# Optimization experiments

Measured on AMD Instinct MI355X. Metric: run time of the kernel, lower is better.

The kernel has to match this reference:

```python
import jax, jax.numpy as jnp
import numpy as np
from jax import lax

N_STEPS = 8          # fixed-step discretization of t in [0, 1]
GN_GROUPS = 32       # group_norm(width) -> GroupNorm(min(32, width), width)
GN_EPS = 1e-5

# Tsit5 Butcher tableau (c nodes, a stage coeffs, b solution weights; b7 = 0)
_C = (0.161, 0.327, 0.9, 0.9800255409045097, 1.0)
_A = (
    (0.161,),
    (-0.008480655492356989, 0.335480655492357),
    (2.8971530571054935, -6.359448489975075, 4.3622954328695815),
    (5.325864828439257, -11.748883564062828, 7.4955393428898365, -0.09249506636175525),
    (5.86145544294642, -12.92096931784711, 8.159367898576159, -0.071584973281401, -0.028269050394068383),
)
_B = (0.09646076681806523, 0.01, 0.4798896504144996, 1.379008574103742, -3.290069515436081, 2.324710524099774)


def _conv3x3(x, w, b):
    # x: [B, Cin, H, W], w: [Cout, Cin, 3, 3], padding=1, stride=1
    y = lax.conv_general_dilated(x, w, (1, 1), ((1, 1), (1, 1)),
                                 dimension_numbers=("NCHW", "OIHW", "NCHW"))
    return y + b[None, :, None, None]


def _group_norm(x, scale, bias):
    B, C, H, W = x.shape
    xr = x.reshape(B, GN_GROUPS, C // GN_GROUPS, H, W)
    mu = xr.mean(axis=(2, 3, 4), keepdims=True)
    var = xr.var(axis=(2, 3, 4), keepdims=True)
    xn = ((xr - mu) * lax.rsqrt(var + GN_EPS)).reshape(B, C, H, W)
    return xn * scale[None, :, None, None] + bias[None, :, None, None]


def _ode_func(t, x, p):
    # ConcatConv2D: prepend a channel filled with scalar t
    B, _, H, W = x.shape
    tt = jnp.full((B, 1, H, W), t, dtype=x.dtype)
    h = _conv3x3(jnp.concatenate([tt, x], axis=1), p["conv1_w"], p["conv1_b"])
    h = jax.nn.relu(_group_norm(h, p["gn1_scale"], p["gn1_bias"]))
    tt2 = jnp.full((B, 1, H, W), t, dtype=x.dtype)
    h = _conv3x3(jnp.concatenate([tt2, h], axis=1), p["conv2_w"], p["conv2_b"])
    return _group_norm(h, p["gn2_scale"], p["gn2_bias"])


def _tsit5_solve(x, p):
    dt = jnp.float32(1.0 / N_STEPS)

    def step(carry, _):
        y, t = carry
        k1 = _ode_func(t, y, p)
        k2 = _ode_func(t + _C[0] * dt, y + dt * (_A[0][0] * k1), p)
        k3 = _ode_func(t + _C[1] * dt, y + dt * (_A[1][0] * k1 + _A[1][1] * k2), p)
        k4 = _ode_func(t + _C[2] * dt,
                       y + dt * (_A[2][0] * k1 + _A[2][1] * k2 + _A[2][2] * k3), p)
        k5 = _ode_func(t + _C[3] * dt,
                       y + dt * (_A[3][0] * k1 + _A[3][1] * k2 + _A[3][2] * k3 + _A[3][3] * k4), p)
        k6 = _ode_func(t + _C[4] * dt,
                       y + dt * (_A[4][0] * k1 + _A[4][1] * k2 + _A[4][2] * k3
                                 + _A[4][3] * k4 + _A[4][4] * k5), p)
        y_next = y + dt * (_B[0] * k1 + _B[1] * k2 + _B[2] * k3
                           + _B[3] * k4 + _B[4] * k5 + _B[5] * k6)
        return (y_next, t + dt), None

    (yT, _), _ = lax.scan(step, (x, jnp.float32(0.0)), None, length=N_STEPS)
    return yT


def setup_inputs() -> dict:
    key = jax.random.key(0)
    ks = jax.random.split(key, 5)
    B, C, H, W = 64, 64, 32, 32
    cin = C + 1  # concat t channel
    fan_in = cin * 9
    lim = 1.0 / np.sqrt(fan_in)
    x = jax.random.normal(ks[0], (B, C, H, W), dtype=jnp.float32)
    conv1_w = jax.random.uniform(ks[1], (C, cin, 3, 3), jnp.float32, -lim, lim)
    conv1_b = jax.random.uniform(ks[2], (C,), jnp.float32, -lim, lim)
    conv2_w = jax.random.uniform(ks[3], (C, cin, 3, 3), jnp.float32, -lim, lim)
    conv2_b = jax.random.uniform(ks[4], (C,), jnp.float32, -lim, lim)
    return {
        "x": x,
        "conv1_w": conv1_w, "conv1_b": conv1_b,
        "gn1_scale": jnp.ones((C,), jnp.float32), "gn1_bias": jnp.zeros((C,), jnp.float32),
        "conv2_w": conv2_w, "conv2_b": conv2_b,
        "gn2_scale": jnp.ones((C,), jnp.float32), "gn2_bias": jnp.zeros((C,), jnp.float32),
    }


def reference(x, conv1_w, conv1_b, gn1_scale, gn1_bias, conv2_w, conv2_b, gn2_scale, gn2_bias):
    p = {"conv1_w": conv1_w, "conv1_b": conv1_b, "gn1_scale": gn1_scale, "gn1_bias": gn1_bias,
         "conv2_w": conv2_w, "conv2_b": conv2_b, "gn2_scale": gn2_scale, "gn2_bias": gn2_bias}
    return _tsit5_solve(x, p)
```

## Files before the change

### kernel.cpp

```cpp
#include <hip/hip_runtime.h>

typedef __attribute__((ext_vector_type(8))) _Float16 f16x8;
typedef __attribute__((ext_vector_type(4))) float f32x4;
typedef unsigned short u16;

#define BB 64
#define NPIX 1024
#define NELEM (BB*64*NPIX)
#define NRT 8

#define PLANE (6*34*64)

__device__ __forceinline__ int swz8(int c8, int p) {
    return (c8 + ((p + (p >> 2)) & 7)) & 7;
}

__device__ __forceinline__ u16 f2h(float x) {
    _Float16 h = (_Float16)x;
    return __builtin_bit_cast(u16, h);
}
__device__ __forceinline__ float h2f(u16 u) {
    return (float)__builtin_bit_cast(_Float16, u);
}

__global__ __launch_bounds__(256) void prep_w_k(
    const float* __restrict__ w, u16* __restrict__ wt)
{
    int t = blockIdx.x*256 + threadIdx.x;
    if (t >= 4608) return;
    int lane = t & 63;
    int f = t >> 6;
    int g = f & 7;
    int tap = f >> 3;
    int coutblk = g & 3;
    int kc = g >> 2;
    int cout = coutblk*16 + (lane & 15);
    int quad = lane >> 4;
    u16 v[8];
#pragma unroll
    for (int j = 0; j < 8; ++j) {
        int cin = kc*32 + quad*8 + j;
        v[j] = f2h(w[((size_t)cout*65 + (cin+1))*9 + tap]);
    }
    u16* dst = wt + ((size_t)tap*4096 + (g*64 + lane)*8);
    *(ushort4*)(dst)     = make_ushort4(v[0], v[1], v[2], v[3]);
    *(ushort4*)(dst + 4) = make_ushort4(v[4], v[5], v[6], v[7]);
}

__global__ __launch_bounds__(256) void smap_k(
    const float* __restrict__ w, float* __restrict__ smap)
{
    int t = blockIdx.x*256 + threadIdx.x;
    int cout = t >> 10;
    int pix = t & 1023;
    int y = pix >> 5, x = pix & 31;
    float s = 0.f;
#pragma unroll
    for (int dy = 0; dy < 3; ++dy)
#pragma unroll
        for (int dx = 0; dx < 3; ++dx) {
            int yy = y + dy - 1, xx = x + dx - 1;
            if ((unsigned)yy < 32u && (unsigned)xx < 32u)
                s += w[(size_t)cout*65*9 + dy*3 + dx];
        }
    smap[t] = s;
}

template<int MODE, int NK, bool WRITEY>
__global__ __launch_bounds__(512, 4) void conv_mfma_k(
    const float* __restrict__ src0, const u16* __restrict__ srcb,
    const u16* __restrict__ kp0, const u16* __restrict__ kp1,
    const u16* __restrict__ kp2, const u16* __restrict__ kp3,
    const u16* __restrict__ kp4, const u16* __restrict__ kp5,
    float* __restrict__ yout,
    float* __restrict__ part,
    const float* __restrict__ gns, const float* __restrict__ gnb,
    const float* __restrict__ gks, const float* __restrict__ gkb,
    const u16* __restrict__ wt, const float* __restrict__ smap,
    const float* __restrict__ bias, u16* __restrict__ out, float tval,
    int slot_in, int slot_out,
    float a1, float a2, float a3, float a4, float a5, float a6)
{
    __shared__ u16 lds_in[PLANE];
    __shared__ float kaf[6][64];
    __shared__ float kbf[64];
    __shared__ float ps[256], pss[256];
    __shared__ float rg[64], rgq[64];

    const int rt  = blockIdx.x;
    const int b   = blockIdx.y;
    const int tid = threadIdx.x;
    const int wv   = tid >> 6;
    const int lane = tid & 63;
    const int quad = lane >> 4;
    const int n15  = lane & 15;
    const int r0   = wv & 3;
    const int mh   = wv >> 2;

    float4 Y0[2], Y1[2];
    ushort4 H0[2], H1[2];

    auto prim_load = [&](int h) {
#pragma unroll
        for (int uu = 0; uu < 2; ++uu) {
            int ur = tid + uu*512;
            if (ur >= 768) continue;
            int u = h*768 + ur;
            int q4 = u & 7;
            int t2 = u >> 3;
            int rr = t2 % 6;
            int c2 = t2 / 6;
            int gr = rt*4 + rr - 1;
            if ((unsigned)gr < 32u) {
                const size_t base = (((size_t)b*64 + c2*2)*32 + gr)*32 + q4*4;
                if constexpr (MODE == 2) {
                    H0[uu] = *(const ushort4*)(srcb + base);
                    H1[uu] = *(const ushort4*)(srcb + base + 1024);
                } else {
                    Y0[uu] = *(const float4*)(src0 + base);
                    Y1[uu] = *(const float4*)(src0 + base + 1024);
                }
            }
        }
    };

    auto stage_finish = [&](int h) {
#pragma unroll
        for (int uu = 0; uu < 2; ++uu) {
            int ur = tid + uu*512;
            if (ur >= 768) continue;
            int u = h*768 + ur;
            int q4 = u & 7;
            int t2 = u >> 3;
            int rr = t2 % 6;
            int c2 = t2 / 6;
            int gr = rt*4 + rr - 1;
            bool ok = (unsigned)gr < 32u;
            int ch0 = c2*2, ch1 = ch0 + 1;
            float4 a0 = make_float4(0.f,0.f,0.f,0.f), a1v = a0;
            if (ok) {
                const size_t base = (((size_t)b*64 + ch0)*32 + gr)*32 + q4*4;
                if constexpr (MODE == 2) {
                    float A0 = kaf[0][ch0], B0 = kbf[ch0];
                    float A1 = kaf[0][ch1], B1 = kbf[ch1];
                    a0.x = fmaxf(fmaf(h2f(H0[uu].x),A0,B0), 0.f);
                    a0.y = fmaxf(fmaf(h2f(H0[uu].y),A0,B0), 0.f);
                    a0.z = fmaxf(fmaf(h2f(H0[uu].z),A0,B0), 0.f);
                    a0.w = fmaxf(fmaf(h2f(H0[uu].w),A0,B0), 0.f);
                    a1v.x = fmaxf(fmaf(h2f(H1[uu].x),A1,B1), 0.f);
                    a1v.y = fmaxf(fmaf(h2f(H1[uu].y),A1,B1), 0.f);
                    a1v.z = fmaxf(fmaf(h2f(H1[uu].z),A1,B1), 0.f);
                    a1v.w = fmaxf(fmaf(h2f(H1[uu].w),A1,B1), 0.f);
                } else {
                    a0 = Y0[uu]; a1v = Y1[uu];
                    if constexpr (MODE == 1) {
                        float f0 = kbf[ch0], f1 = kbf[ch1];
                        a0.x += f0; a0.y += f0; a0.z += f0; a0.w += f0;
                        a1v.x += f1; a1v.y += f1; a1v.z += f1; a1v.w += f1;
                        const u16* kps[6] = {kp0, kp1, kp2, kp3, kp4, kp5};
#pragma unroll
                        for (int jj = 0; jj < NK; ++jj) {
                            ushort4 kv0 = *(const ushort4*)(kps[jj] + base);
                            ushort4 kv1 = *(const ushort4*)(kps[jj] + base + 1024);
                            float fa0 = kaf[jj][ch0], fa1 = kaf[jj][ch1];
                            a0.x = fmaf(fa0, h2f(kv0.x), a0.x);
                            a0.y = fmaf(fa0, h2f(kv0.y), a0.y);
                            a0.z = fmaf(fa0, h2f(kv0.z), a0.z);
                            a0.w = fmaf(fa0, h2f(kv0.w), a0.w);
                            a1v.x = fmaf(fa1, h2f(kv1.x), a1v.x);
                            a1v.y = fmaf(fa1, h2f(kv1.y), a1v.y);
                            a1v.z = fmaf(fa1, h2f(kv1.z), a1v.z);
                            a1v.w = fmaf(fa1, h2f(kv1.w), a1v.w);
                        }
                    }
                }
                if constexpr (WRITEY) {
                    if (rr >= 1 && rr <= 4) {
                        *(float4*)(yout + base)        = a0;
                        *(float4*)(yout + base + 1024) = a1v;
                    }
                }
            }
            float v0[4] = {a0.x, a0.y, a0.z, a0.w};
            float v1[4] = {a1v.x, a1v.y, a1v.z, a1v.w};
            int c8 = c2 >> 2, cl = c2 & 3;
            int pbase = rr*34 + 1 + q4*4;
#pragma unroll
            for (int j = 0; j < 4; ++j) {
                int p = pbase + j;
                int au = p*64 + swz8(c8, p)*8 + cl*2;
                *(unsigned*)&lds_in[au] =
                    (unsigned)f2h(v0[j]) | ((unsigned)f2h(v1[j]) << 16);
            }
        }
    };

    f32x4 acc[2][2] = {};
    auto mfma_kc = [&](int kc) {
#pragma unroll 3
        for (int tap = 0; tap < 9; ++tap) {
            const int dy = tap / 3;
            const int dx = tap - dy*3;
            const int rowoff = (r0 + dy)*34 + dx;
            const u16* wtap = wt + (size_t)tap*4096;
            f16x8 A[2], Bf[2];
#pragma unroll
            for (int mt = 0; mt < 2; ++mt)
                A[mt] = *(const f16x8*)
                    &wtap[((kc*4 + mh*2 + mt)*64 + lane)*8];
#pragma unroll
            for (int nt = 0; nt < 2; ++nt) {
                int p = rowoff + nt*16 + n15;
                Bf[nt] = *(const f16x8*)&lds_in[p*64 + swz8(kc*4 + quad, p)*8];
            }
#pragma unroll
            for (int mt = 0; mt < 2; ++mt)
#pragma unroll
                for (int nt = 0; nt < 2; ++nt)
                    acc[mt][nt] = __builtin_amdgcn_mfma_f32_16x16x32_f16(
                        A[mt], Bf[nt], acc[mt][nt], 0, 0, 0);
        }
    };

    prim_load(0);

    if constexpr (MODE == 1) {
        if (tid < 64) {
            const float aa[6] = {a1, a2, a3, a4, a5, a6};
            int g = tid >> 1;
            float acb = 0.f;
#pragma unroll
            for (int jj = 0; jj < NK; ++jj) {
                const float4* pp = (const float4*)
                    (part + ((((size_t)(1+jj)*64 + b)*32 + g)*NRT)*2);
                float4 x0 = pp[0], x1 = pp[1], x2 = pp[2], x3 = pp[3];
                float S  = x0.x+x0.z + x1.x+x1.z + x2.x+x2.z + x3.x+x3.z;
                float SS = x0.y+x0.w + x1.y+x1.w + x2.y+x2.w + x3.y+x3.w;
                float mu   = S * (1.f/2048.f);
                float var  = SS * (1.f/2048.f) - mu*mu;
                float rstd = rsqrtf(var + 1e-5f);
                float a = gks[tid]*rstd;
                float c = gkb[tid] - mu*a;
                kaf[jj][tid] = aa[jj]*a;
                acb += aa[jj]*c;
            }
            kbf[tid] = acb;
        }
    } else if constexpr (MODE == 2) {
        if (tid < 64) {
            int g = tid >> 1;
            const float4* pp = (const float4*)
                (part + ((((size_t)slot_in*64 + b)*32 + g)*NRT)*2);
            float4 x0 = pp[0], x1 = pp[1], x2 = pp[2], x3 = pp[3];
            float S  = x0.x+x0.z + x1.x+x1.z + x2.x+x2.z + x3.x+x3.z;
            float SS = x0.y+x0.w + x1.y+x1.w + x2.y+x2.w + x3.y+x3.w;
            float mu   = S * (1.f/2048.f);
            float var  = SS * (1.f/2048.f) - mu*mu;
            float rstd = rsqrtf(var + 1e-5f);
            float a = gns[tid]*rstd;
            kaf[0][tid] = a;
            kbf[tid] = gnb[tid] - mu*a;
        }
    }
    __syncthreads();

    stage_finish(0);
    if (tid < 384) {
        int c2 = tid & 31;
        int t3 = tid >> 5;
        int rr = t3 % 6;
        int e  = t3 / 6;
        int p  = rr*34 + e*33;
        int au = p*64 + swz8(c2 >> 2, p)*8 + (c2 & 3)*2;
        *(unsigned*)&lds_in[au] = 0u;
    }
    __syncthreads();

    prim_load(1);
    mfma_kc(0);
    stage_finish(1);
    __syncthreads();

    mfma_kc(1);

    const int orow = rt*4 + r0;
#pragma unroll
    for (int mt = 0; mt < 2; ++mt) {
#pragma unroll
        for (int r = 0; r < 4; ++r) {
            int cout = mh*32 + mt*16 + quad*4 + r;
            float bs = bias[cout];
            const float* sp = smap + (size_t)cout*1024 + orow*32;
            u16* op = out + (((size_t)b*64 + cout)*32 + orow)*32;
            float v0 = acc[mt][0][r] + bs + tval*sp[n15];
            float v1 = acc[mt][1][r] + bs + tval*sp[16 + n15];
            op[n15]      = f2h(v0);
            op[16 + n15] = f2h(v1);
            float s = v0 + v1;
            float q = v0*v0 + v1*v1;
            s += __shfl_xor(s, 1); q += __shfl_xor(q, 1);
            s += __shfl_xor(s, 2); q += __shfl_xor(q, 2);
            s += __shfl_xor(s, 4); q += __shfl_xor(q, 4);
            s += __shfl_xor(s, 8); q += __shfl_xor(q, 8);
            if (n15 == 0) { ps[r0*64 + cout] = s; pss[r0*64 + cout] = q; }
        }
    }
    __syncthreads();
    if (tid < 64) {
        rg[tid]  = ps[tid]  + ps[64+tid]  + ps[128+tid]  + ps[192+tid];
        rgq[tid] = pss[tid] + pss[64+tid] + pss[128+tid] + pss[192+tid];
    }
    __syncthreads();
    if (tid < 32) {
        float S  = rg[2*tid]  + rg[2*tid+1];
        float SS = rgq[2*tid] + rgq[2*tid+1];
        float* pp = part + ((((size_t)slot_out*64 + b)*32 + tid)*NRT + rt)*2;
        pp[0] = S; pp[1] = SS;
    }
}

__global__ __launch_bounds__(256) void final_combine_k(
    const float* __restrict__ ysrc, float* __restrict__ ydst,
    const u16* __restrict__ k0, const u16* __restrict__ k1,
    const u16* __restrict__ k2, const u16* __restrict__ k3,
    const u16* __restrict__ k4, const u16* __restrict__ k5,
    const float* __restrict__ part,
    const float* __restrict__ g2s, const float* __restrict__ g2b,
    float b0, float b1, float b2, float b3, float b4, float b5)
{
    const int bidx = blockIdx.x;
    const int b = bidx >> 6, ch = bidx & 63, g = ch >> 1;
    const int t = threadIdx.x;
    __shared__ float rs[6][2];
    if (t < 12) {
        int jj = t >> 1, st = t & 1;
        const float* pp = part + ((((size_t)(1+jj)*64 + b)*32 + g)*NRT)*2 + st;
        float v = 0.f;
#pragma unroll
        for (int q = 0; q < NRT; ++q) v += pp[2*q];
        rs[jj][st] = v;
    }
    __syncthreads();
    const float bb[6] = {b0, b1, b2, b3, b4, b5};
    float fa[6], fcs = 0.f;
#pragma unroll
    for (int jj = 0; jj < 6; ++jj) {
        float mu   = rs[jj][0] * (1.f/2048.f);
        float var  = rs[jj][1] * (1.f/2048.f) - mu*mu;
        float rstd = rsqrtf(var + 1e-5f);
        float a = g2s[ch]*rstd;
        float c = g2b[ch] - mu*a;
        fa[jj] = bb[jj]*a;
        fcs   += bb[jj]*c;
    }
    const size_t base = ((size_t)bidx*256 + t)*4;
    float4 r = *(const float4*)(ysrc + base);
    r.x += fcs; r.y += fcs; r.z += fcs; r.w += fcs;
    const u16* kp[6] = {k0, k1, k2, k3, k4, k5};
#pragma unroll
    for (int jj = 0; jj < 6; ++jj) {
        ushort4 kv = *(const ushort4*)(kp[jj] + base);
        r.x = fmaf(fa[jj], h2f(kv.x), r.x);
        r.y = fmaf(fa[jj], h2f(kv.y), r.y);
        r.z = fmaf(fa[jj], h2f(kv.z), r.z);
        r.w = fmaf(fa[jj], h2f(kv.w), r.w);
    }
    *(float4*)(ydst + base) = r;
}


static const double A_[5][5] = {
    {0.161, 0, 0, 0, 0},
    {-0.008480655492356989, 0.335480655492357, 0, 0, 0},
    {2.8971530571054935, -6.359448489975075, 4.3622954328695815, 0, 0},
    {5.325864828439257, -11.748883564062828, 7.4955393428898365, -0.09249506636175525, 0},
    {5.86145544294642, -12.92096931784711, 8.159367898576159, -0.071584973281401, -0.028269050394068383},
};
static const double B_[6] = {
    0.09646076681806523, 0.01, 0.4798896504144996,
    1.379008574103742, -3.290069515436081, 2.324710524099774,
};
static const double C_[5] = {0.161, 0.327, 0.9, 0.9800255409045097, 1.0};

extern "C" void kernel_launch(void* const* d_in, const int* in_sizes, int n_in,
                              void* d_out, int out_size, void* d_ws, size_t ws_size,
                              hipStream_t stream)
{
    const float* x   = (const float*)d_in[0];
    const float* c1w = (const float*)d_in[1];
    const float* c1b = (const float*)d_in[2];
    const float* g1s = (const float*)d_in[3];
    const float* g1b = (const float*)d_in[4];
    const float* c2w = (const float*)d_in[5];
    const float* c2b = (const float*)d_in[6];
    const float* g2s = (const float*)d_in[7];
    const float* g2b = (const float*)d_in[8];

    float* y  = (float*)d_out;
    u16*   wsb = (u16*)d_ws;
    u16*   h  = wsb;
    u16*   k[6];
    for (int i = 0; i < 6; ++i) k[i] = wsb + (size_t)(1 + i) * NELEM;
    u16*   wt1   = wsb + (size_t)7*NELEM;
    u16*   wt2   = wt1 + 73728;
    float* smap1 = (float*)(wt2 + 73728);
    float* smap2 = smap1 + 65536;
    float* part  = smap2 + 65536;
    float* YA    = part + (size_t)7*64*32*8*2;
    float* YB    = YA + NELEM;
    float* yb[2] = {YA, YB};

    const double dt = 0.125;
    const float dtf = 0.125f;

    prep_w_k<<<18, 256, 0, stream>>>(c1w, wt1);
    prep_w_k<<<18, 256, 0, stream>>>(c2w, wt2);
    smap_k<<<256, 256, 0, stream>>>(c1w, smap1);
    smap_k<<<256, 256, 0, stream>>>(c2w, smap2);

    hipMemcpyAsync(YA, x, (size_t)NELEM * sizeof(float),
                   hipMemcpyDeviceToDevice, stream);

    const dim3 cgrid(NRT, BB);
    const float bw0 = (float)(B_[0]*dt), bw1 = (float)(B_[1]*dt),
                bw2 = (float)(B_[2]*dt), bw3 = (float)(B_[3]*dt),
                bw4 = (float)(B_[4]*dt), bw5 = (float)(B_[5]*dt);

    for (int s = 0; s < 8; ++s) {
        const float t0 = dtf * (float)s;
        const float* ys = yb[s & 1];

        if (s == 0) {
            conv_mfma_k<0,0,false><<<cgrid, 512, 0, stream>>>(
                YA, nullptr, nullptr,nullptr,nullptr,nullptr,nullptr,nullptr,
                nullptr, part, g1s, g1b, g2s, g2b,
                wt1, smap1, c1b, h, t0, 0, 0,
                0.f,0.f,0.f,0.f,0.f,0.f);
        } else {
            conv_mfma_k<1,6,true><<<cgrid, 512, 0, stream>>>(
                yb[(s-1)&1], nullptr, k[0],k[1],k[2],k[3],k[4],k[5],
                yb[s&1], part, g1s, g1b, g2s, g2b,
                wt1, smap1, c1b, h, t0, 0, 0,
                bw0, bw1, bw2, bw3, bw4, bw5);
        }
        conv_mfma_k<2,0,false><<<cgrid, 512, 0, stream>>>(
            nullptr, h, nullptr,nullptr,nullptr,nullptr,nullptr,nullptr,
            nullptr, part, g1s, g1b, g2s, g2b,
            wt2, smap2, c2b, k[0], t0, 0, 1,
            0.f,0.f,0.f,0.f,0.f,0.f);

        for (int j = 1; j < 6; ++j) {
            const float tj = t0 + (float)C_[j-1] * dtf;
            float a[5] = {0,0,0,0,0};
            for (int i = 0; i < j; ++i) a[i] = (float)(A_[j-1][i] * dt);
            switch (j) {
            case 1:
                conv_mfma_k<1,1,false><<<cgrid, 512, 0, stream>>>(
                    ys, nullptr, k[0],k[1],k[2],k[3],k[4],k[5],
                    nullptr, part, g1s, g1b, g2s, g2b,
                    wt1, smap1, c1b, h, tj, 0, 0,
                    a[0],a[1],a[2],a[3],a[4],0.f); break;
            case 2:
                conv_mfma_k<1,2,false><<<cgrid, 512, 0, stream>>>(
                    ys, nullptr, k[0],k[1],k[2],k[3],k[4],k[5],
                    nullptr, part, g1s, g1b, g2s, g2b,
                    wt1, smap1, c1b, h, tj, 0, 0,
                    a[0],a[1],a[2],a[3],a[4],0.f); break;
            case 3:
                conv_mfma_k<1,3,false><<<cgrid, 512, 0, stream>>>(
                    ys, nullptr, k[0],k[1],k[2],k[3],k[4],k[5],
                    nullptr, part, g1s, g1b, g2s, g2b,
                    wt1, smap1, c1b, h, tj, 0, 0,
                    a[0],a[1],a[2],a[3],a[4],0.f); break;
            case 4:
                conv_mfma_k<1,4,false><<<cgrid, 512, 0, stream>>>(
                    ys, nullptr, k[0],k[1],k[2],k[3],k[4],k[5],
                    nullptr, part, g1s, g1b, g2s, g2b,
                    wt1, smap1, c1b, h, tj, 0, 0,
                    a[0],a[1],a[2],a[3],a[4],0.f); break;
            default:
                conv_mfma_k<1,5,false><<<cgrid, 512, 0, stream>>>(
                    ys, nullptr, k[0],k[1],k[2],k[3],k[4],k[5],
                    nullptr, part, g1s, g1b, g2s, g2b,
                    wt1, smap1, c1b, h, tj, 0, 0,
                    a[0],a[1],a[2],a[3],a[4],0.f); break;
            }
            conv_mfma_k<2,0,false><<<cgrid, 512, 0, stream>>>(
                nullptr, h, nullptr,nullptr,nullptr,nullptr,nullptr,nullptr,
                nullptr, part, g1s, g1b, g2s, g2b,
                wt2, smap2, c2b, k[j], tj, 0, 1 + j,
                0.f,0.f,0.f,0.f,0.f,0.f);
        }
    }
    final_combine_k<<<4096, 256, 0, stream>>>(
        yb[7 & 1], y, k[0], k[1], k[2], k[3], k[4], k[5], part, g2s, g2b,
        bw0, bw1, bw2, bw3, bw4, bw5);
}
```

Before: 1.835 ms.

## Store RK stage derivatives in fp32 and use 256-thread conv blocks when workspace allows

Adds a conv32_k path that writes the stage derivatives k[j] as fp32 instead of fp16, with the stage-combination and final-combine kernels reading them as float4. The conv kernel drops from 512 to 256 threads per block, each wave covering both output-channel halves with a 2x2x2 accumulator set. The new path is chosen only when the workspace is large enough, and the fp16 path stays as a fallback. The intent appears to be better accuracy and a different work split per wave, at the cost of twice the k-buffer memory traffic.

```diff
diff --git a/kernel.cpp b/kernel.cpp
--- a/kernel.cpp
+++ b/kernel.cpp
@@ -14,7 +14,6 @@
 __device__ __forceinline__ int swz8(int c8, int p) {
     return (c8 + ((p + (p >> 2)) & 7)) & 7;
 }
-
 __device__ __forceinline__ u16 f2h(float x) {
     _Float16 h = (_Float16)x;
     return __builtin_bit_cast(u16, h);
@@ -67,7 +66,320 @@
 }
 
 template<int MODE, int NK, bool WRITEY>
-__global__ __launch_bounds__(512, 4) void conv_mfma_k(
+__global__ __launch_bounds__(256, 4) void conv32_k(
+    const float* __restrict__ src0, const u16* __restrict__ srcb,
+    const float* __restrict__ kp0, const float* __restrict__ kp1,
+    const float* __restrict__ kp2, const float* __restrict__ kp3,
+    const float* __restrict__ kp4, const float* __restrict__ kp5,
+    float* __restrict__ yout,
+    float* __restrict__ part,
+    const float* __restrict__ gns, const float* __restrict__ gnb,
+    const float* __restrict__ gks, const float* __restrict__ gkb,
+    const u16* __restrict__ wt, const float* __restrict__ smap,
+    const float* __restrict__ bias, u16* __restrict__ outh,
+    float* __restrict__ outk, float tval,
+    int slot_in, int slot_out,
+    float a1, float a2, float a3, float a4, float a5, float a6)
+{
+    __shared__ u16 lds_in[PLANE];
+    __shared__ float kaf[6][64];
+    __shared__ float kbf[64];
+    __shared__ float ps[256], pss[256];
+    __shared__ float rg[64], rgq[64];
+
+    const int rt  = blockIdx.x;
+    const int b   = blockIdx.y;
+    const int tid = threadIdx.x;
+    const int wv   = tid >> 6;
+    const int lane = tid & 63;
+    const int quad = lane >> 4;
+    const int n15  = lane & 15;
+    const int r0   = wv;
+
+    float4 Y0[3], Y1[3];
+    ushort4 H0[3], H1[3];
+
+    auto prim_load = [&](int hh) {
+#pragma unroll
+        for (int uu = 0; uu < 3; ++uu) {
+            int u = hh*768 + tid + uu*256;
+            int q4 = u & 7;
+            int t2 = u >> 3;
+            int rr = t2 % 6;
+            int c2 = t2 / 6;
+            int gr = rt*4 + rr - 1;
+            if ((unsigned)gr < 32u) {
+                const size_t base = (((size_t)b*64 + c2*2)*32 + gr)*32 + q4*4;
+                if constexpr (MODE == 2) {
+                    H0[uu] = *(const ushort4*)(srcb + base);
+                    H1[uu] = *(const ushort4*)(srcb + base + 1024);
+                } else {
+                    Y0[uu] = *(const float4*)(src0 + base);
+                    Y1[uu] = *(const float4*)(src0 + base + 1024);
+                }
+            }
+        }
+    };
+
+    auto stage_finish = [&](int hh) {
+#pragma unroll
+        for (int uu = 0; uu < 3; ++uu) {
+            int u = hh*768 + tid + uu*256;
+            int q4 = u & 7;
+            int t2 = u >> 3;
+            int rr = t2 % 6;
+            int c2 = t2 / 6;
+            int gr = rt*4 + rr - 1;
+            bool ok = (unsigned)gr < 32u;
+            int ch0 = c2*2, ch1 = ch0 + 1;
+            float4 a0 = make_float4(0.f,0.f,0.f,0.f), a1v = a0;
+            if (ok) {
+                const size_t base = (((size_t)b*64 + ch0)*32 + gr)*32 + q4*4;
+                if constexpr (MODE == 2) {
+                    float A0 = kaf[0][ch0], B0 = kbf[ch0];
+                    float A1 = kaf[0][ch1], B1 = kbf[ch1];
+                    a0.x = fmaxf(fmaf(h2f(H0[uu].x),A0,B0), 0.f);
+                    a0.y = fmaxf(fmaf(h2f(H0[uu].y),A0,B0), 0.f);
+                    a0.z = fmaxf(fmaf(h2f(H0[uu].z),A0,B0), 0.f);
+                    a0.w = fmaxf(fmaf(h2f(H0[uu].w),A0,B0), 0.f);
+                    a1v.x = fmaxf(fmaf(h2f(H1[uu].x),A1,B1), 0.f);
+                    a1v.y = fmaxf(fmaf(h2f(H1[uu].y),A1,B1), 0.f);
+                    a1v.z = fmaxf(fmaf(h2f(H1[uu].z),A1,B1), 0.f);
+                    a1v.w = fmaxf(fmaf(h2f(H1[uu].w),A1,B1), 0.f);
+                } else {
+                    a0 = Y0[uu]; a1v = Y1[uu];
+                    if constexpr (MODE == 1) {
+                        float f0 = kbf[ch0], f1 = kbf[ch1];
+                        a0.x += f0; a0.y += f0; a0.z += f0; a0.w += f0;
+                        a1v.x += f1; a1v.y += f1; a1v.z += f1; a1v.w += f1;
+                        const float* kps[6] = {kp0, kp1, kp2, kp3, kp4, kp5};
+#pragma unroll
+                        for (int jj = 0; jj < NK; ++jj) {
+                            float4 kv0 = *(const float4*)(kps[jj] + base);
+                            float4 kv1 = *(const float4*)(kps[jj] + base + 1024);
+                            float fa0 = kaf[jj][ch0], fa1 = kaf[jj][ch1];
+                            a0.x = fmaf(fa0, kv0.x, a0.x);
+                            a0.y = fmaf(fa0, kv0.y, a0.y);
+                            a0.z = fmaf(fa0, kv0.z, a0.z);
+                            a0.w = fmaf(fa0, kv0.w, a0.w);
+                            a1v.x = fmaf(fa1, kv1.x, a1v.x);
+                            a1v.y = fmaf(fa1, kv1.y, a1v.y);
+                            a1v.z = fmaf(fa1, kv1.z, a1v.z);
+                            a1v.w = fmaf(fa1, kv1.w, a1v.w);
+                        }
+                    }
+                }
+                if constexpr (WRITEY) {
+                    if (rr >= 1 && rr <= 4) {
+                        *(float4*)(yout + base)        = a0;
+                        *(float4*)(yout + base + 1024) = a1v;
+                    }
+                }
+            }
+            float v0[4] = {a0.x, a0.y, a0.z, a0.w};
+            float v1[4] = {a1v.x, a1v.y, a1v.z, a1v.w};
+            int c8 = c2 >> 2, cl = c2 & 3;
+            int pbase = rr*34 + 1 + q4*4;
+#pragma unroll
+            for (int j = 0; j < 4; ++j) {
+                int p = pbase + j;
+                int au = p*64 + swz8(c8, p)*8 + cl*2;
+                *(unsigned*)&lds_in[au] =
+                    (unsigned)f2h(v0[j]) | ((unsigned)f2h(v1[j]) << 16);
+            }
+        }
+    };
+
+    f32x4 acc[2][2][2] = {};
+    auto mfma_kc = [&](int kc) {
+#pragma unroll 3
+        for (int tap = 0; tap < 9; ++tap) {
+            const int dy = tap / 3;
+            const int dx = tap - dy*3;
+            const int rowoff = (r0 + dy)*34 + dx;
+            const u16* wtap = wt + (size_t)tap*4096;
+            f16x8 Bf[2];
+#pragma unroll
+            for (int nt = 0; nt < 2; ++nt) {
+                int p = rowoff + nt*16 + n15;
+                Bf[nt] = *(const f16x8*)&lds_in[p*64 + swz8(kc*4 + quad, p)*8];
+            }
+#pragma unroll
+            for (int mh = 0; mh < 2; ++mh) {
+                f16x8 A0 = *(const f16x8*)&wtap[((kc*4 + mh*2 + 0)*64 + lane)*8];
+                f16x8 A1 = *(const f16x8*)&wtap[((kc*4 + mh*2 + 1)*64 + lane)*8];
+#pragma unroll
+                for (int nt = 0; nt < 2; ++nt) {
+                    acc[mh][0][nt] = __builtin_amdgcn_mfma_f32_16x16x32_f16(
+                        A0, Bf[nt], acc[mh][0][nt], 0, 0, 0);
+                    acc[mh][1][nt] = __builtin_amdgcn_mfma_f32_16x16x32_f16(
+                        A1, Bf[nt], acc[mh][1][nt], 0, 0, 0);
+                }
+            }
+        }
+    };
+
+    prim_load(0);
+
+    if constexpr (MODE == 1) {
+        if (tid < 64) {
+            const float aa[6] = {a1, a2, a3, a4, a5, a6};
+            int g = tid >> 1;
+            float acb = 0.f;
+#pragma unroll
+            for (int jj = 0; jj < NK; ++jj) {
+                const float4* pp = (const float4*)
+                    (part + ((((size_t)(1+jj)*64 + b)*32 + g)*NRT)*2);
+                float4 x0 = pp[0], x1 = pp[1], x2 = pp[2], x3 = pp[3];
+                float S  = x0.x+x0.z + x1.x+x1.z + x2.x+x2.z + x3.x+x3.z;
+                float SS = x0.y+x0.w + x1.y+x1.w + x2.y+x2.w + x3.y+x3.w;
+                float mu   = S * (1.f/2048.f);
+                float var  = SS * (1.f/2048.f) - mu*mu;
+                float rstd = rsqrtf(var + 1e-5f);
+                float a = gks[tid]*rstd;
+                float c = gkb[tid] - mu*a;
+                kaf[jj][tid] = aa[jj]*a;
+                acb += aa[jj]*c;
+            }
+            kbf[tid] = acb;
+        }
+    } else if constexpr (MODE == 2) {
+        if (tid < 64) {
+            int g = tid >> 1;
+            const float4* pp = (const float4*)
+                (part + ((((size_t)slot_in*64 + b)*32 + g)*NRT)*2);
+            float4 x0 = pp[0], x1 = pp[1], x2 = pp[2], x3 = pp[3];
+            float S  = x0.x+x0.z + x1.x+x1.z + x2.x+x2.z + x3.x+x3.z;
+            float SS = x0.y+x0.w + x1.y+x1.w + x2.y+x2.w + x3.y+x3.w;
+            float mu   = S * (1.f/2048.f);
+            float var  = SS * (1.f/2048.f) - mu*mu;
+            float rstd = rsqrtf(var + 1e-5f);
+            float a = gns[tid]*rstd;
+            kaf[0][tid] = a;
+            kbf[tid] = gnb[tid] - mu*a;
+        }
+    }
+    __syncthreads();
+
+    stage_finish(0);
+#pragma unroll
+    for (int i = 0; i < 2; ++i) {
+        int u = tid + i*256;
+        if (u < 384) {
+            int c2 = u & 31;
+            int t3 = u >> 5;
+            int rr = t3 % 6;
+            int e  = t3 / 6;
+            int p  = rr*34 + e*33;
+            int au = p*64 + swz8(c2 >> 2, p)*8 + (c2 & 3)*2;
+            *(unsigned*)&lds_in[au] = 0u;
+        }
+    }
+    __syncthreads();
+
+    prim_load(1);
+    mfma_kc(0);
+    stage_finish(1);
+    __syncthreads();
+
+    mfma_kc(1);
+
+    const int orow = rt*4 + r0;
+#pragma unroll
+    for (int mh = 0; mh < 2; ++mh) {
+#pragma unroll
+        for (int mt = 0; mt < 2; ++mt) {
+#pragma unroll
+            for (int r = 0; r < 4; ++r) {
+                int cout = mh*32 + mt*16 + quad*4 + r;
+                float bs = bias[cout];
+                const float* sp = smap + (size_t)cout*1024 + orow*32;
+                float v0 = acc[mh][mt][0][r] + bs + tval*sp[n15];
+                float v1 = acc[mh][mt][1][r] + bs + tval*sp[16 + n15];
+                if constexpr (MODE == 2) {
+                    float* op = outk + (((size_t)b*64 + cout)*32 + orow)*32;
+                    op[n15]      = v0;
+                    op[16 + n15] = v1;
+                } else {
+                    u16* op = outh + (((size_t)b*64 + cout)*32 + orow)*32;
+                    op[n15]      = f2h(v0);
+                    op[16 + n15] = f2h(v1);
+                }
+                float s = v0 + v1;
+                float q = v0*v0 + v1*v1;
+                s += __shfl_xor(s, 1); q += __shfl_xor(q, 1);
+                s += __shfl_xor(s, 2); q += __shfl_xor(q, 2);
+                s += __shfl_xor(s, 4); q += __shfl_xor(q, 4);
+                s += __shfl_xor(s, 8); q += __shfl_xor(q, 8);
+                if (n15 == 0) { ps[r0*64 + cout] = s; pss[r0*64 + cout] = q; }
+            }
+        }
+    }
+    __syncthreads();
+    if (tid < 64) {
+        rg[tid]  = ps[tid]  + ps[64+tid]  + ps[128+tid]  + ps[192+tid];
+        rgq[tid] = pss[tid] + pss[64+tid] + pss[128+tid] + pss[192+tid];
+    }
+    __syncthreads();
+    if (tid < 32) {
+        float S  = rg[2*tid]  + rg[2*tid+1];
+        float SS = rgq[2*tid] + rgq[2*tid+1];
+        float* pp = part + ((((size_t)slot_out*64 + b)*32 + tid)*NRT + rt)*2;
+        pp[0] = S; pp[1] = SS;
+    }
+}
+
+__global__ __launch_bounds__(256) void final_combine32_k(
+    const float* __restrict__ ysrc, float* __restrict__ ydst,
+    const float* __restrict__ k0, const float* __restrict__ k1,
+    const float* __restrict__ k2, const float* __restrict__ k3,
+    const float* __restrict__ k4, const float* __restrict__ k5,
+    const float* __restrict__ part,
+    const float* __restrict__ g2s, const float* __restrict__ g2b,
+    float b0, float b1, float b2, float b3, float b4, float b5)
+{
+    const int bidx = blockIdx.x;
+    const int b = bidx >> 6, ch = bidx & 63, g = ch >> 1;
+    const int t = threadIdx.x;
+    __shared__ float rs[6][2];
+    if (t < 12) {
+        int jj = t >> 1, st = t & 1;
+        const float* pp = part + ((((size_t)(1+jj)*64 + b)*32 + g)*NRT)*2 + st;
+        float v = 0.f;
+#pragma unroll
+        for (int q = 0; q < NRT; ++q) v += pp[2*q];
+        rs[jj][st] = v;
+    }
+    __syncthreads();
+    const float bb[6] = {b0, b1, b2, b3, b4, b5};
+    float fa[6], fcs = 0.f;
+#pragma unroll
+    for (int jj = 0; jj < 6; ++jj) {
+        float mu   = rs[jj][0] * (1.f/2048.f);
+        float var  = rs[jj][1] * (1.f/2048.f) - mu*mu;
+        float rstd = rsqrtf(var + 1e-5f);
+        float a = g2s[ch]*rstd;
+        float c = g2b[ch] - mu*a;
+        fa[jj] = bb[jj]*a;
+        fcs   += bb[jj]*c;
+    }
+    const size_t base = ((size_t)bidx*256 + t)*4;
+    float4 r = *(const float4*)(ysrc + base);
+    r.x += fcs; r.y += fcs; r.z += fcs; r.w += fcs;
+    const float* kp[6] = {k0, k1, k2, k3, k4, k5};
+#pragma unroll
+    for (int jj = 0; jj < 6; ++jj) {
+        float4 kv = *(const float4*)(kp[jj] + base);
+        r.x = fmaf(fa[jj], kv.x, r.x);
+        r.y = fmaf(fa[jj], kv.y, r.y);
+        r.z = fmaf(fa[jj], kv.z, r.z);
+        r.w = fmaf(fa[jj], kv.w, r.w);
+    }
+    *(float4*)(ydst + base) = r;
+}
+
+template<int MODE, int NK, bool WRITEY>
+__global__ __launch_bounds__(512, 4) void conv16_k(
     const float* __restrict__ src0, const u16* __restrict__ srcb,
     const u16* __restrict__ kp0, const u16* __restrict__ kp1,
     const u16* __restrict__ kp2, const u16* __restrict__ kp3,
@@ -100,12 +412,12 @@
     float4 Y0[2], Y1[2];
     ushort4 H0[2], H1[2];
 
-    auto prim_load = [&](int h) {
+    auto prim_load = [&](int hh) {
 #pragma unroll
         for (int uu = 0; uu < 2; ++uu) {
             int ur = tid + uu*512;
             if (ur >= 768) continue;
-            int u = h*768 + ur;
+            int u = hh*768 + ur;
             int q4 = u & 7;
             int t2 = u >> 3;
             int rr = t2 % 6;
@@ -124,12 +436,12 @@
         }
     };
 
-    auto stage_finish = [&](int h) {
+    auto stage_finish = [&](int hh) {
 #pragma unroll
         for (int uu = 0; uu < 2; ++uu) {
             int ur = tid + uu*512;
             if (ur >= 768) continue;
-            int u = h*768 + ur;
+            int u = hh*768 + ur;
             int q4 = u & 7;
             int t2 = u >> 3;
             int rr = t2 % 6;
@@ -319,7 +631,7 @@
     }
 }
 
-__global__ __launch_bounds__(256) void final_combine_k(
+__global__ __launch_bounds__(256) void final_combine16_k(
     const float* __restrict__ ysrc, float* __restrict__ ydst,
     const u16* __restrict__ k0, const u16* __restrict__ k1,
     const u16* __restrict__ k2, const u16* __restrict__ k3,
@@ -398,101 +710,196 @@
 
     float* y  = (float*)d_out;
     u16*   wsb = (u16*)d_ws;
-    u16*   h  = wsb;
-    u16*   k[6];
-    for (int i = 0; i < 6; ++i) k[i] = wsb + (size_t)(1 + i) * NELEM;
-    u16*   wt1   = wsb + (size_t)7*NELEM;
-    u16*   wt2   = wt1 + 73728;
-    float* smap1 = (float*)(wt2 + 73728);
-    float* smap2 = smap1 + 65536;
-    float* part  = smap2 + 65536;
-    float* YA    = part + (size_t)7*64*32*8*2;
-    float* YB    = YA + NELEM;
-    float* yb[2] = {YA, YB};
 
     const double dt = 0.125;
     const float dtf = 0.125f;
-
-    prep_w_k<<<18, 256, 0, stream>>>(c1w, wt1);
-    prep_w_k<<<18, 256, 0, stream>>>(c2w, wt2);
-    smap_k<<<256, 256, 0, stream>>>(c1w, smap1);
-    smap_k<<<256, 256, 0, stream>>>(c2w, smap2);
-
-    hipMemcpyAsync(YA, x, (size_t)NELEM * sizeof(float),
-                   hipMemcpyDeviceToDevice, stream);
-
-    const dim3 cgrid(NRT, BB);
     const float bw0 = (float)(B_[0]*dt), bw1 = (float)(B_[1]*dt),
                 bw2 = (float)(B_[2]*dt), bw3 = (float)(B_[3]*dt),
                 bw4 = (float)(B_[4]*dt), bw5 = (float)(B_[5]*dt);
-
-    for (int s = 0; s < 8; ++s) {
-        const float t0 = dtf * (float)s;
-        const float* ys = yb[s & 1];
-
-        if (s == 0) {
-            conv_mfma_k<0,0,false><<<cgrid, 512, 0, stream>>>(
-                YA, nullptr, nullptr,nullptr,nullptr,nullptr,nullptr,nullptr,
-                nullptr, part, g1s, g1b, g2s, g2b,
-                wt1, smap1, c1b, h, t0, 0, 0,
-                0.f,0.f,0.f,0.f,0.f,0.f);
-        } else {
-            conv_mfma_k<1,6,true><<<cgrid, 512, 0, stream>>>(
-                yb[(s-1)&1], nullptr, k[0],k[1],k[2],k[3],k[4],k[5],
-                yb[s&1], part, g1s, g1b, g2s, g2b,
-                wt1, smap1, c1b, h, t0, 0, 0,
-                bw0, bw1, bw2, bw3, bw4, bw5);
-        }
-        conv_mfma_k<2,0,false><<<cgrid, 512, 0, stream>>>(
-            nullptr, h, nullptr,nullptr,nullptr,nullptr,nullptr,nullptr,
-            nullptr, part, g1s, g1b, g2s, g2b,
-            wt2, smap2, c2b, k[0], t0, 0, 1,
-            0.f,0.f,0.f,0.f,0.f,0.f);
-
-        for (int j = 1; j < 6; ++j) {
-            const float tj = t0 + (float)C_[j-1] * dtf;
-            float a[5] = {0,0,0,0,0};
-            for (int i = 0; i < j; ++i) a[i] = (float)(A_[j-1][i] * dt);
-            switch (j) {
-            case 1:
-                conv_mfma_k<1,1,false><<<cgrid, 512, 0, stream>>>(
-                    ys, nullptr, k[0],k[1],k[2],k[3],k[4],k[5],
+    const dim3 cgrid(NRT, BB);
+
+    const size_t need32 =
+        (size_t)NELEM*2 + (size_t)6*NELEM*4 + (size_t)2*73728*2
+      + (size_t)2*65536*4 + (size_t)7*64*32*NRT*2*4 + (size_t)2*NELEM*4;
+
+    if (ws_size >= need32) {
+        u16*   h    = wsb;
+        float* kf   = (float*)(wsb + (size_t)NELEM);
+        float* k[6];
+        for (int i = 0; i < 6; ++i) k[i] = kf + (size_t)i*NELEM;
+        u16*   wt1   = (u16*)(kf + (size_t)6*NELEM);
+        u16*   wt2   = wt1 + 73728;
+        float* smap1 = (float*)(wt2 + 73728);
+        float* smap2 = smap1 + 65536;
+        float* part  = smap2 + 65536;
+        float* YA    = part + (size_t)7*64*32*NRT*2;
+        float* YB    = YA + NELEM;
+        float* yb[2] = {YA, YB};
+
+        prep_w_k<<<18, 256, 0, stream>>>(c1w, wt1);
+        prep_w_k<<<18, 256, 0, stream>>>(c2w, wt2);
+        smap_k<<<256, 256, 0, stream>>>(c1w, smap1);
+        smap_k<<<256, 256, 0, stream>>>(c2w, smap2);
+        hipMemcpyAsync(YA, x, (size_t)NELEM * sizeof(float),
+                       hipMemcpyDeviceToDevice, stream);
+
+        for (int s = 0; s < 8; ++s) {
+            const float t0 = dtf * (float)s;
+            const float* ys = yb[s & 1];
+
+            if (s == 0) {
+                conv32_k<0,0,false><<<cgrid, 256, 0, stream>>>(
+                    YA, nullptr, nullptr,nullptr,nullptr,nullptr,nullptr,nullptr,
                     nullptr, part, g1s, g1b, g2s, g2b,
-                    wt1, smap1, c1b, h, tj, 0, 0,
-                    a[0],a[1],a[2],a[3],a[4],0.f); break;
-            case 2:
-                conv_mfma_k<1,2,false><<<cgrid, 512, 0, stream>>>(
-                    ys, nullptr, k[0],k[1],k[2],k[3],k[4],k[5],
-                    nullptr, part, g1s, g1b, g2s, g2b,
-                    wt1, smap1, c1b, h, tj, 0, 0,
-                    a[0],a[1],a[2],a[3],a[4],0.f); break;
-            case 3:
-                conv_mfma_k<1,3,false><<<cgrid, 512, 0, stream>>>(
-                    ys, nullptr, k[0],k[1],k[2],k[3],k[4],k[5],
-                    nullptr, part, g1s, g1b, g2s, g2b,
-                    wt1, smap1, c1b, h, tj, 0, 0,
-                    a[0],a[1],a[2],a[3],a[4],0.f); break;
-            case 4:
-                conv_mfma_k<1,4,false><<<cgrid, 512, 0, stream>>>(
-                    ys, nullptr, k[0],k[1],k[2],k[3],k[4],k[5],
-                    nullptr, part, g1s, g1b, g2s, g2b,
-                    wt1, smap1, c1b, h, tj, 0, 0,
-                    a[0],a[1],a[2],a[3],a[4],0.f); break;
-            default:
-                conv_mfma_k<1,5,false><<<cgrid, 512, 0, stream>>>(
-                    ys, nullptr, k[0],k[1],k[2],k[3],k[4],k[5],
-                    nullptr, part, g1s, g1b, g2s, g2b,
-                    wt1, smap1, c1b, h, tj, 0, 0,
-                    a[0],a[1],a[2],a[3],a[4],0.f); break;
-            }
-            conv_mfma_k<2,0,false><<<cgrid, 512, 0, stream>>>(
+                    wt1, smap1, c1b, h, nullptr, t0, 0, 0,
+                    0.f,0.f,0.f,0.f,0.f,0.f);
+            } else {
+                conv32_k<1,6,true><<<cgrid, 256, 0, stream>>>(
+                    yb[(s-1)&1], nullptr, k[0],k[1],k[2],k[3],k[4],k[5],
+                    yb[s&1], part, g1s, g1b, g2s, g2b,
+                    wt1, smap1, c1b, h, nullptr, t0, 0, 0,
+                    bw0, bw1, bw2, bw3, bw4, bw5);
+            }
+            conv32_k<2,0,false><<<cgrid, 256, 0, stream>>>(
                 nullptr, h, nullptr,nullptr,nullptr,nullptr,nullptr,nullptr,
                 nullptr, part, g1s, g1b, g2s, g2b,
-                wt2, smap2, c2b, k[j], tj, 0, 1 + j,
+                wt2, smap2, c2b, nullptr, k[0], t0, 0, 1,
                 0.f,0.f,0.f,0.f,0.f,0.f);
-        }
-    }
-    final_combine_k<<<4096, 256, 0, stream>>>(
-        yb[7 & 1], y, k[0], k[1], k[2], k[3], k[4], k[5], part, g2s, g2b,
-        bw0, bw1, bw2, bw3, bw4, bw5);
+
+            for (int j = 1; j < 6; ++j) {
+                const float tj = t0 + (float)C_[j-1] * dtf;
+                float a[5] = {0,0,0,0,0};
+                for (int i = 0; i < j; ++i) a[i] = (float)(A_[j-1][i] * dt);
+                switch (j) {
+                case 1:
+                    conv32_k<1,1,false><<<cgrid, 256, 0, stream>>>(
+                        ys, nullptr, k[0],k[1],k[2],k[3],k[4],k[5],
+                        nullptr, part, g1s, g1b, g2s, g2b,
+                        wt1, smap1, c1b, h, nullptr, tj, 0, 0,
+                        a[0],a[1],a[2],a[3],a[4],0.f); break;
+                case 2:
+                    conv32_k<1,2,false><<<cgrid, 256, 0, stream>>>(
+                        ys, nullptr, k[0],k[1],k[2],k[3],k[4],k[5],
+                        nullptr, part, g1s, g1b, g2s, g2b,
+                        wt1, smap1, c1b, h, nullptr, tj, 0, 0,
+                        a[0],a[1],a[2],a[3],a[4],0.f); break;
+                case 3:
+                    conv32_k<1,3,false><<<cgrid, 256, 0, stream>>>(
+                        ys, nullptr, k[0],k[1],k[2],k[3],k[4],k[5],
+                        nullptr, part, g1s, g1b, g2s, g2b,
+                        wt1, smap1, c1b, h, nullptr, tj, 0, 0,
+                        a[0],a[1],a[2],a[3],a[4],0.f); break;
+                case 4:
+                    conv32_k<1,4,false><<<cgrid, 256, 0, stream>>>(
+                        ys, nullptr, k[0],k[1],k[2],k[3],k[4],k[5],
+                        nullptr, part, g1s, g1b, g2s, g2b,
+                        wt1, smap1, c1b, h, nullptr, tj, 0, 0,
+                        a[0],a[1],a[2],a[3],a[4],0.f); break;
+                default:
+                    conv32_k<1,5,false><<<cgrid, 256, 0, stream>>>(
+                        ys, nullptr, k[0],k[1],k[2],k[3],k[4],k[5],
+                        nullptr, part, g1s, g1b, g2s, g2b,
+                        wt1, smap1, c1b, h, nullptr, tj, 0, 0,
+                        a[0],a[1],a[2],a[3],a[4],0.f); break;
+                }
+                conv32_k<2,0,false><<<cgrid, 256, 0, stream>>>(
+                    nullptr, h, nullptr,nullptr,nullptr,nullptr,nullptr,nullptr,
+                    nullptr, part, g1s, g1b, g2s, g2b,
+                    wt2, smap2, c2b, nullptr, k[j], tj, 0, 1 + j,
+                    0.f,0.f,0.f,0.f,0.f,0.f);
+            }
+        }
+        final_combine32_k<<<4096, 256, 0, stream>>>(
+            yb[7 & 1], y, k[0], k[1], k[2], k[3], k[4], k[5], part, g2s, g2b,
+            bw0, bw1, bw2, bw3, bw4, bw5);
+    } else {
+        u16*   h  = wsb;
+        u16*   k[6];
+        for (int i = 0; i < 6; ++i) k[i] = wsb + (size_t)(1 + i) * NELEM;
+        u16*   wt1   = wsb + (size_t)7*NELEM;
+        u16*   wt2   = wt1 + 73728;
+        float* smap1 = (float*)(wt2 + 73728);
+        float* smap2 = smap1 + 65536;
+        float* part  = smap2 + 65536;
+        float* YA    = part + (size_t)7*64*32*NRT*2;
+        float* YB    = YA + NELEM;
+        float* yb[2] = {YA, YB};
+
+        prep_w_k<<<18, 256, 0, stream>>>(c1w, wt1);
+        prep_w_k<<<18, 256, 0, stream>>>(c2w, wt2);
+        smap_k<<<256, 256, 0, stream>>>(c1w, smap1);
+        smap_k<<<256, 256, 0, stream>>>(c2w, smap2);
+        hipMemcpyAsync(YA, x, (size_t)NELEM * sizeof(float),
+                       hipMemcpyDeviceToDevice, stream);
+
+        for (int s = 0; s < 8; ++s) {
+            const float t0 = dtf * (float)s;
+            const float* ys = yb[s & 1];
+
+            if (s == 0) {
+                conv16_k<0,0,false><<<cgrid, 512, 0, stream>>>(
+                    YA, nullptr, nullptr,nullptr,nullptr,nullptr,nullptr,nullptr,
+                    nullptr, part, g1s, g1b, g2s, g2b,
+                    wt1, smap1, c1b, h, t0, 0, 0,
+                    0.f,0.f,0.f,0.f,0.f,0.f);
+            } else {
+                conv16_k<1,6,true><<<cgrid, 512, 0, stream>>>(
+                    yb[(s-1)&1], nullptr, k[0],k[1],k[2],k[3],k[4],k[5],
+                    yb[s&1], part, g1s, g1b, g2s, g2b,
+                    wt1, smap1, c1b, h, t0, 0, 0,
+                    bw0, bw1, bw2, bw3, bw4, bw5);
+            }
+            conv16_k<2,0,false><<<cgrid, 512, 0, stream>>>(
+                nullptr, h, nullptr,nullptr,nullptr,nullptr,nullptr,nullptr,
+                nullptr, part, g1s, g1b, g2s, g2b,
+                wt2, smap2, c2b, k[0], t0, 0, 1,
+                0.f,0.f,0.f,0.f,0.f,0.f);
+
+            for (int j = 1; j < 6; ++j) {
+                const float tj = t0 + (float)C_[j-1] * dtf;
+                float a[5] = {0,0,0,0,0};
+                for (int i = 0; i < j; ++i) a[i] = (float)(A_[j-1][i] * dt);
+                switch (j) {
+                case 1:
+                    conv16_k<1,1,false><<<cgrid, 512, 0, stream>>>(
+                        ys, nullptr, k[0],k[1],k[2],k[3],k[4],k[5],
+                        nullptr, part, g1s, g1b, g2s, g2b,
+                        wt1, smap1, c1b, h, tj, 0, 0,
+                        a[0],a[1],a[2],a[3],a[4],0.f); break;
+                case 2:
+                    conv16_k<1,2,false><<<cgrid, 512, 0, stream>>>(
+                        ys, nullptr, k[0],k[1],k[2],k[3],k[4],k[5],
+                        nullptr, part, g1s, g1b, g2s, g2b,
+                        wt1, smap1, c1b, h, tj, 0, 0,
+                        a[0],a[1],a[2],a[3],a[4],0.f); break;
+                case 3:
+                    conv16_k<1,3,false><<<cgrid, 512, 0, stream>>>(
+                        ys, nullptr, k[0],k[1],k[2],k[3],k[4],k[5],
+                        nullptr, part, g1s, g1b, g2s, g2b,
+                        wt1, smap1, c1b, h, tj, 0, 0,
+                        a[0],a[1],a[2],a[3],a[4],0.f); break;
+                case 4:
+                    conv16_k<1,4,false><<<cgrid, 512, 0, stream>>>(
+                        ys, nullptr, k[0],k[1],k[2],k[3],k[4],k[5],
+                        nullptr, part, g1s, g1b, g2s, g2b,
+                        wt1, smap1, c1b, h, tj, 0, 0,
+                        a[0],a[1],a[2],a[3],a[4],0.f); break;
+                default:
+                    conv16_k<1,5,false><<<cgrid, 512, 0, stream>>>(
+                        ys, nullptr, k[0],k[1],k[2],k[3],k[4],k[5],
+                        nullptr, part, g1s, g1b, g2s, g2b,
+                        wt1, smap1, c1b, h, tj, 0, 0,
+                        a[0],a[1],a[2],a[3],a[4],0.f); break;
+                }
+                conv16_k<2,0,false><<<cgrid, 512, 0, stream>>>(
+                    nullptr, h, nullptr,nullptr,nullptr,nullptr,nullptr,nullptr,
+                    nullptr, part, g1s, g1b, g2s, g2b,
+                    wt2, smap2, c2b, k[j], tj, 0, 1 + j,
+                    0.f,0.f,0.f,0.f,0.f,0.f);
+            }
+        }
+        final_combine16_k<<<4096, 256, 0, stream>>>(
+            yb[7 & 1], y, k[0], k[1], k[2], k[3], k[4], k[5], part, g2s, g2b,
+            bw0, bw1, bw2, bw3, bw4, bw5);
+    }
 }
```

After: 3.145 ms. 1.71x slower.
